# Kernel optimization log

Hardware: AMD Instinct MI355X
Metric: run time of the kernel (lower is better)

The kernel has to match this reference:

```python
import jax, jax.numpy as jnp
import numpy as np

HIDDEN = 768
HEADS = 12
HEAD_DIM = 64
SEQ = 512
DS_K = 64  # downsampling_k
EPS = 1e-6


def setup_inputs() -> dict:
    key = jax.random.key(0)
    ks = jax.random.split(key, 16)
    B = 32
    sd = 1.0 / DS_K
    glorot = jax.nn.initializers.lecun_normal()  # flax default_kernel_init
    inp = {
        "query": jax.random.normal(ks[0], (B, SEQ, HIDDEN), jnp.float32),
        "key": jax.random.normal(ks[1], (B, SEQ, HIDDEN), jnp.float32),
        "value": jax.random.normal(ks[2], (B, SEQ, HIDDEN), jnp.float32),
        "step": 0,
        # learned Linformer-style downsampling projections [k, s]
        "W_kds": sd * jax.random.normal(ks[3], (DS_K, SEQ), jnp.float32),
        "W_vds": sd * jax.random.normal(ks[4], (DS_K, SEQ), jnp.float32),
        # DenseGeneral qkv kernels [d, n, h] and biases [n, h]
        "Wq": glorot(ks[5], (HIDDEN, HEADS, HEAD_DIM), jnp.float32),
        "bq": jnp.zeros((HEADS, HEAD_DIM), jnp.float32),
        "Wk": glorot(ks[6], (HIDDEN, HEADS, HEAD_DIM), jnp.float32),
        "bk": jnp.zeros((HEADS, HEAD_DIM), jnp.float32),
        "Wv": glorot(ks[7], (HIDDEN, HEADS, HEAD_DIM), jnp.float32),
        "bv": jnp.zeros((HEADS, HEAD_DIM), jnp.float32),
        # out projection contracts (n, h) -> hidden
        "Wout": glorot(ks[8], (HEADS * HEAD_DIM, HIDDEN), jnp.float32).reshape(HEADS, HEAD_DIM, HIDDEN),
        "bout": jnp.zeros((HIDDEN,), jnp.float32),
    }
    return inp


def reference(query, key, value, step, W_kds, W_vds, Wq, bq, Wk, bk, Wv, bv, Wout, bout):
    # Linformer-style downsample of keys/values along sequence: [b,s,d] -> [b,k,d]
    key_ds = jnp.einsum("ks,bsd->bkd", W_kds, key)
    val_ds = jnp.einsum("ks,bsd->bkd", W_vds, value)

    # per-head projections
    queries = jnp.einsum("bqd,dnh->bqnh", query, Wq) + bq    # [b,q,n,h]
    keys = jnp.einsum("bkd,dnh->bknh", key_ds, Wk) + bk      # [b,k,n,h]
    values = jnp.einsum("bkd,dnh->bknh", val_ds, Wv) + bv    # [b,k,n,h]

    # kernelized linear attention with elu feature map (mask=False path)
    phi_q = jax.nn.elu(queries) + 1.0
    phi_k = jax.nn.elu(keys) + 1.0
    s = jnp.einsum("bknd,bknh->bndh", phi_k, values)          # [b,n,h,h] KV state
    z = jnp.sum(phi_k, axis=1)                                 # [b,n,h]
    qs = jnp.einsum("bqnd,bndh->bqnh", phi_q, s)
    qz = jnp.einsum("bqnd,bnd->bqn", phi_q, z) + EPS
    a_v = qs / qz[..., None]                                   # [b,q,n,h]

    out = jnp.einsum("bqnh,nhD->bqD", a_v, Wout) + bout        # [b,q,hidden]
    return out
```

## Files before the change

### kernel.cpp

```cpp
#include <hip/hip_runtime.h>

typedef unsigned short u16;
typedef u16 u16x8 __attribute__((ext_vector_type(8)));
typedef __bf16 bf16;
typedef bf16 bf16x8 __attribute__((ext_vector_type(8)));
typedef float f32x4 __attribute__((ext_vector_type(4)));

__device__ __forceinline__ float bf2f(u16 v) {
  union { unsigned u; float f; } x; x.u = ((unsigned)v) << 16; return x.f;
}
__device__ __forceinline__ u16 f2bf(float f) {
  union { float f; unsigned u; } x; x.f = f;
  unsigned u = x.u;
  u += 0x7fffu + ((u >> 16) & 1u);
  return (u16)(u >> 16);
}

#define GLDS16(g, l) __builtin_amdgcn_global_load_lds( \
    (const __attribute__((address_space(1))) unsigned int*)(const void*)(g), \
    (__attribute__((address_space(3))) unsigned int*)(void*)(l), 16, 0, 0)

__global__ __launch_bounds__(256) void prep_k(
    const float* __restrict__ Wq, const float* __restrict__ Wk,
    const float* __restrict__ Wv, const float* __restrict__ Wout,
    const float* __restrict__ query,
    const float* __restrict__ wkds, const float* __restrict__ wvds,
    const float* __restrict__ b0, const float* __restrict__ b1,
    const float* __restrict__ b2, const float* __restrict__ b3,
    u16* __restrict__ WT, u16* __restrict__ q_bf,
    u16* __restrict__ dstW, u16* __restrict__ dstB)
{
  __shared__ u16 T[64][72];
  const int blk = blockIdx.x;
  const int t = threadIdx.x;
  if (blk < 576) {
    const int bz = blk / 144, rr = blk % 144;
    const int r0 = (rr / 12) * 64, c0 = (rr % 12) * 64;
    const float* W = (bz == 0) ? Wq : (bz == 1) ? Wk : (bz == 2) ? Wv : Wout;
    u16* O = WT + (size_t)bz * 768 * 768;
    #pragma unroll
    for (int p = 0; p < 2; ++p) {
      int v = t + p * 256;
      int r = v / 8, c = (v % 8) * 8;
      f32x4 x0 = *(const f32x4*)&W[(size_t)(r0 + r) * 768 + c0 + c];
      f32x4 x1 = *(const f32x4*)&W[(size_t)(r0 + r) * 768 + c0 + c + 4];
      #pragma unroll
      for (int i = 0; i < 4; ++i) { T[r][c + i] = f2bf(x0[i]); T[r][c + 4 + i] = f2bf(x1[i]); }
    }
    __syncthreads();
    #pragma unroll
    for (int p = 0; p < 2; ++p) {
      int v = t + p * 256;
      int r = v / 8, c = (v % 8) * 8;
      u16x8 tv;
      #pragma unroll
      for (int i = 0; i < 8; ++i) tv[i] = T[c + i][r];
      *(u16x8*)&O[(size_t)(c0 + r) * 768 + r0 + c] = tv;
    }
  } else if (blk < 6720) {
    const size_t i = (size_t)(blk - 576) * 256 + t;
    f32x4 a = *(const f32x4*)&query[i * 8];
    f32x4 b = *(const f32x4*)&query[i * 8 + 4];
    u16x8 w;
    #pragma unroll
    for (int j = 0; j < 4; ++j) { w[j] = f2bf(a[j]); w[4 + j] = f2bf(b[j]); }
    *(u16x8*)&q_bf[i * 8] = w;
  } else {
    const int i = (blk - 6720) * 256 + t;
    if (i < 32768)      dstW[i] = f2bf(wkds[i]);
    else if (i < 65536) dstW[i] = f2bf(wvds[i - 32768]);
    else {
      int j = i - 65536, s = j / 768, si = j % 768;
      const float* src = (s == 0) ? b0 : (s == 1) ? b1 : (s == 2) ? b2 : b3;
      dstB[j] = f2bf(src[si]);
    }
  }
}

__global__ __launch_bounds__(256) void ds_k(
    const u16* __restrict__ Wds,
    const float* __restrict__ key, const float* __restrict__ value,
    u16* __restrict__ key_ds)
{
  __shared__ u16 Bs[2][64 * 40];
  const int pair = blockIdx.y >> 5, b = blockIdx.y & 31;
  const float* src = (pair ? value : key) + (size_t)b * 512 * 768;
  const u16* W = Wds + pair * 32768;
  u16* dst = key_ds + (size_t)pair * 1572864 + (size_t)b * 49152;
  const int nt = blockIdx.x * 64;
  const int t = threadIdx.x, wave = t >> 6, lane = t & 63;
  const int wm = (wave >> 1) * 32, wn = (wave & 1) * 32;
  const int lrow = lane & 15, quad = lane >> 4;
  const int bn = t & 63, bk8 = (t >> 6) * 8;
  const float* bcol = src + nt + bn;

  f32x4 acc[2][2] = {};
  float breg[8];
  bf16x8 av[2][2];

  #pragma unroll
  for (int i = 0; i < 8; ++i) breg[i] = bcol[(size_t)(bk8 + i) * 768];
  #pragma unroll
  for (int i = 0; i < 2; ++i)
    av[0][i] = *(const bf16x8*)&W[(size_t)(wm + i * 16 + lrow) * 512 + quad * 8];

  #pragma unroll
  for (int step = 0; step < 16; ++step) {
    const int cur = step & 1, nxt = cur ^ 1;
    u16x8 wv;
    #pragma unroll
    for (int i = 0; i < 8; ++i) wv[i] = f2bf(breg[i]);
    *(u16x8*)&Bs[cur][bn * 40 + bk8] = wv;
    if (step < 15) {
      const int k1 = (step + 1) * 32;
      #pragma unroll
      for (int i = 0; i < 8; ++i) breg[i] = bcol[(size_t)(k1 + bk8 + i) * 768];
      #pragma unroll
      for (int i = 0; i < 2; ++i)
        av[nxt][i] = *(const bf16x8*)&W[(size_t)(wm + i * 16 + lrow) * 512 + k1 + quad * 8];
    }
    __syncthreads();
    bf16x8 bv[2];
    #pragma unroll
    for (int j = 0; j < 2; ++j)
      bv[j] = *(const bf16x8*)&Bs[cur][(wn + j * 16 + lrow) * 40 + quad * 8];
    #pragma unroll
    for (int i = 0; i < 2; ++i)
      #pragma unroll
      for (int j = 0; j < 2; ++j)
        acc[i][j] = __builtin_amdgcn_mfma_f32_16x16x32_bf16(av[cur][i], bv[j], acc[i][j], 0, 0, 0);
  }

  #pragma unroll
  for (int i = 0; i < 2; ++i)
    #pragma unroll
    for (int j = 0; j < 2; ++j) {
      const int col = nt + wn + j * 16 + lrow;
      #pragma unroll
      for (int r = 0; r < 4; ++r) {
        const int row = wm + i * 16 + quad * 4 + r;
        dst[(size_t)row * 768 + col] = f2bf(acc[i][j][r]);
      }
    }
}

template<int ACT, bool OF32>
__global__ __launch_bounds__(256) void gemm97_k(
    const u16* __restrict__ A, int lda,
    const u16* __restrict__ Bt, int ldb,
    void* __restrict__ Craw, int ldc,
    const u16* __restrict__ bias, int K)
{
  __shared__ u16 As[128 * 32];
  __shared__ u16 Bs[128 * 32];
  const int mt = blockIdx.x * 128, nt = blockIdx.y * 128;
  const int t = threadIdx.x, wave = t >> 6, lane = t & 63;
  const int wm = (wave >> 1) * 64, wn = (wave & 1) * 64;
  const int lrow = lane & 15, quad = lane >> 4;
  f32x4 acc[4][4] = {};

  for (int k0 = 0; k0 < K; k0 += 32) {
    __syncthreads();
    #pragma unroll
    for (int p = 0; p < 2; ++p) {
      const int s = wave * 128 + p * 64 + lane;
      const int r = s >> 2, c = (s & 3) * 8;
      const int lb = (wave * 128 + p * 64) * 8;
      GLDS16(&A[(size_t)(mt + r) * lda + k0 + c], &As[lb]);
      GLDS16(&Bt[(size_t)(nt + r) * ldb + k0 + c], &Bs[lb]);
    }
    __syncthreads();

    bf16x8 av[4], bv[4];
    #pragma unroll
    for (int i = 0; i < 4; ++i) av[i] = *(const bf16x8*)&As[(wm + i * 16 + lrow) * 32 + quad * 8];
    #pragma unroll
    for (int j = 0; j < 4; ++j) bv[j] = *(const bf16x8*)&Bs[(wn + j * 16 + lrow) * 32 + quad * 8];
    #pragma unroll
    for (int i = 0; i < 4; ++i)
      #pragma unroll
      for (int j = 0; j < 4; ++j)
        acc[i][j] = __builtin_amdgcn_mfma_f32_16x16x32_bf16(av[i], bv[j], acc[i][j], 0, 0, 0);
  }

  #pragma unroll
  for (int i = 0; i < 4; ++i) {
    #pragma unroll
    for (int j = 0; j < 4; ++j) {
      const int col = nt + wn + j * 16 + lrow;
      const float badd = bias ? bf2f(bias[col]) : 0.0f;
      #pragma unroll
      for (int r = 0; r < 4; ++r) {
        const int row = mt + wm + i * 16 + quad * 4 + r;
        float v = acc[i][j][r] + badd;
        if constexpr (ACT == 1) v = v > 0.0f ? v + 1.0f : __expf(v);
        if constexpr (OF32) ((float*)Craw)[(size_t)row * ldc + col] = v;
        else                ((u16*)Craw)[(size_t)row * ldc + col] = f2bf(v);
      }
    }
  }
}

template<int BM, int BN, int BK, int WM, int WN>
__global__ __launch_bounds__(256) void gemmkv_k(
    const u16* __restrict__ A, int lda,
    const u16* __restrict__ B, int ldb,
    u16* __restrict__ C, int ldc,
    const u16* __restrict__ bias,
    int K,
    long long offA_b, long long offB_b, long long offC_b, long long offBias_b)
{
  constexpr int LDSK = BK + 8;
  __shared__ u16 As[BM][LDSK];
  __shared__ u16 Bs[BN][LDSK];
  const int bb = blockIdx.z;
  A += bb * offA_b; B += bb * offB_b; C += bb * offC_b; bias += bb * offBias_b;
  const int mt = blockIdx.x * BM;
  const int nt = blockIdx.y * BN;
  const int t = threadIdx.x;
  const int wave = t >> 6, lane = t & 63;
  constexpr int WAVES_N = BN / WN;
  const int wm = (wave / WAVES_N) * WM;
  const int wn = (wave % WAVES_N) * WN;
  constexpr int FM = WM / 16, FN = WN / 16;
  const int lrow = lane & 15, quad = lane >> 4;
  f32x4 acc[FM][FN] = {};

  for (int k0 = 0; k0 < K; k0 += BK) {
    __syncthreads();
    #pragma unroll
    for (int p = 0; p < (BM * BK / 8) / 256; ++p) {
      int v = t + p * 256;
      int r = v / (BK / 8), c = (v % (BK / 8)) * 8;
      *(u16x8*)&As[r][c] = *(const u16x8*)&A[(size_t)(mt + r) * lda + k0 + c];
    }
    #pragma unroll
    for (int p = 0; p < (BN * BK / 8) / 256; ++p) {
      int v = t + p * 256;
      int r = v / (BK / 8), c = (v % (BK / 8)) * 8;
      *(u16x8*)&Bs[r][c] = *(const u16x8*)&B[(size_t)(nt + r) * ldb + k0 + c];
    }
    __syncthreads();
    bf16x8 av[FM], bv[FN];
    #pragma unroll
    for (int i = 0; i < FM; ++i) av[i] = *(const bf16x8*)&As[wm + i * 16 + lrow][quad * 8];
    #pragma unroll
    for (int j = 0; j < FN; ++j) bv[j] = *(const bf16x8*)&Bs[wn + j * 16 + lrow][quad * 8];
    #pragma unroll
    for (int i = 0; i < FM; ++i)
      #pragma unroll
      for (int j = 0; j < FN; ++j)
        acc[i][j] = __builtin_amdgcn_mfma_f32_16x16x32_bf16(av[i], bv[j], acc[i][j], 0, 0, 0);
  }
  #pragma unroll
  for (int i = 0; i < FM; ++i)
    #pragma unroll
    for (int j = 0; j < FN; ++j) {
      const int col = nt + wn + j * 16 + lrow;
      const float badd = bf2f(bias[col]);
      #pragma unroll
      for (int r = 0; r < 4; ++r) {
        const int row = mt + wm + i * 16 + quad * 4 + r;
        float v = acc[i][j][r] + badd;
        if (bb == 0) v = v > 0.0f ? v + 1.0f : __expf(v);
        C[(size_t)row * ldc + col] = f2bf(v);
      }
    }
}

__global__ __launch_bounds__(256) void kv_state_k(
    const u16* __restrict__ phi_k, const u16* __restrict__ vals,
    u16* __restrict__ sT, float* __restrict__ z)
{
  __shared__ float pk[64][65];
  __shared__ float vv[64][65];
  const int x = blockIdx.x;
  const int b = x / 12, n = x % 12;
  const int t = threadIdx.x;
  const u16* pkg = phi_k + (size_t)b * 64 * 768 + n * 64;
  const u16* vvg = vals  + (size_t)b * 64 * 768 + n * 64;
  #pragma unroll
  for (int p = 0; p < 2; ++p) {
    int v = t + p * 256;
    int r = v / 8, c = (v % 8) * 8;
    u16x8 a  = *(const u16x8*)&pkg[(size_t)r * 768 + c];
    u16x8 bq = *(const u16x8*)&vvg[(size_t)r * 768 + c];
    #pragma unroll
    for (int i = 0; i < 8; ++i) { pk[r][c + i] = bf2f(a[i]); vv[r][c + i] = bf2f(bq[i]); }
  }
  __syncthreads();
  const int d0 = (t >> 4) * 4, h0 = (t & 15) * 4;
  float s4[4][4] = {};
  for (int k = 0; k < 64; ++k) {
    float pv[4], vb[4];
    #pragma unroll
    for (int i = 0; i < 4; ++i) { pv[i] = pk[k][d0 + i]; vb[i] = vv[k][h0 + i]; }
    #pragma unroll
    for (int i = 0; i < 4; ++i)
      #pragma unroll
      for (int j = 0; j < 4; ++j) s4[i][j] += pv[i] * vb[j];
  }
  const size_t base = (size_t)x * 4096;
  #pragma unroll
  for (int i = 0; i < 4; ++i)
    #pragma unroll
    for (int j = 0; j < 4; ++j)
      sT[base + (size_t)(h0 + j) * 64 + d0 + i] = f2bf(s4[i][j]);
  if (t < 64) {
    float zz = 0.f;
    for (int k = 0; k < 64; ++k) zz += pk[k][t];
    z[(size_t)x * 64 + t] = zz;
  }
}

__global__ __launch_bounds__(256) void attn_av_k(
    u16* __restrict__ phi_q, const u16* __restrict__ sT, const float* __restrict__ zbuf)
{
  __shared__ u16 As[64 * 72];
  __shared__ u16 Bs[64 * 72];
  __shared__ float zv[64];
  __shared__ float zpart[4][64];
  __shared__ float zq[64];
  const int x = blockIdx.x, y = blockIdx.y;
  const int b = y / 12, n = y % 12;
  const int t = threadIdx.x;
  u16* Abase = phi_q + (size_t)b * 512 * 768 + (size_t)x * 64 * 768 + n * 64;
  const u16* Bbase = sT + (size_t)y * 4096;
  if (t < 64) zv[t] = zbuf[(size_t)y * 64 + t];
  #pragma unroll
  for (int p = 0; p < 2; ++p) {
    int v = t + p * 256;
    int r = v >> 3, c = (v & 7) * 8;
    *(u16x8*)&As[r * 72 + c] = *(const u16x8*)&Abase[(size_t)r * 768 + c];
    *(u16x8*)&Bs[r * 72 + c] = *(const u16x8*)&Bbase[r * 64 + c];
  }
  __syncthreads();
  {
    int r = t & 63, seg = t >> 6;
    float s = 0.f;
    #pragma unroll
    for (int j = 0; j < 16; ++j) s += bf2f(As[r * 72 + seg * 16 + j]) * zv[seg * 16 + j];
    zpart[seg][r] = s;
  }
  __syncthreads();
  if (t < 64) {
    float s = zpart[0][t] + zpart[1][t] + zpart[2][t] + zpart[3][t];
    zq[t] = 1.0f / (s + 1e-6f);
  }
  const int wave = t >> 6, lane = t & 63;
  const int wm = (wave >> 1) * 32, wn = (wave & 1) * 32;
  const int lrow = lane & 15, quad = lane >> 4;
  f32x4 acc[2][2] = {};
  #pragma unroll
  for (int c = 0; c < 2; ++c) {
    bf16x8 av[2], bv[2];
    #pragma unroll
    for (int i = 0; i < 2; ++i) av[i] = *(const bf16x8*)&As[(wm + i * 16 + lrow) * 72 + c * 32 + quad * 8];
    #pragma unroll
    for (int j = 0; j < 2; ++j) bv[j] = *(const bf16x8*)&Bs[(wn + j * 16 + lrow) * 72 + c * 32 + quad * 8];
    #pragma unroll
    for (int i = 0; i < 2; ++i)
      #pragma unroll
      for (int j = 0; j < 2; ++j)
        acc[i][j] = __builtin_amdgcn_mfma_f32_16x16x32_bf16(av[i], bv[j], acc[i][j], 0, 0, 0);
  }
  __syncthreads();
  #pragma unroll
  for (int i = 0; i < 2; ++i)
    #pragma unroll
    for (int j = 0; j < 2; ++j) {
      const int col = wn + j * 16 + lrow;
      #pragma unroll
      for (int r = 0; r < 4; ++r) {
        const int row = wm + i * 16 + quad * 4 + r;
        Abase[(size_t)row * 768 + col] = f2bf(acc[i][j][r] * zq[row]);
      }
    }
}

__global__ void tagfill_k(float* out, float val, int n) {
  int i = blockIdx.x * 256 + threadIdx.x;
  if (i < n) out[i] = val;
}

extern "C" void kernel_launch(void* const* d_in, const int* in_sizes, int n_in,
                              void* d_out, int out_size, void* d_ws, size_t ws_size,
                              hipStream_t stream) {
  (void)out_size;
  float* out = (float*)d_out;

  int o;
  if (n_in >= 14 && in_sizes[3] == 1) o = 4;
  else if (n_in == 13) o = 3;
  else { tagfill_k<<<4, 256, 0, stream>>>(out, 77.0f, 1024); return; }
  if (in_sizes[0] != 12582912 || in_sizes[o + 0] != 32768 || in_sizes[o + 2] != 589824) {
    tagfill_k<<<4, 256, 0, stream>>>(out, 88.0f, 1024); return;
  }

  const float* query = (const float*)d_in[0];
  const float* key   = (const float*)d_in[1];
  const float* value = (const float*)d_in[2];
  const float* W_kds = (const float*)d_in[o + 0];
  const float* W_vds = (const float*)d_in[o + 1];
  const float* Wq   = (const float*)d_in[o + 2];
  const float* bq   = (const float*)d_in[o + 3];
  const float* Wk   = (const float*)d_in[o + 4];
  const float* bk   = (const float*)d_in[o + 5];
  const float* Wv   = (const float*)d_in[o + 6];
  const float* bv   = (const float*)d_in[o + 7];
  const float* Wout = (const float*)d_in[o + 8];
  const float* bout = (const float*)d_in[o + 9];

  const size_t NEED = 55187456;
  if (ws_size < NEED) { tagfill_k<<<4, 256, 0, stream>>>(out, 123.0f, 1024); return; }

  char* base = (char*)d_ws;
  u16*   WT     = (u16*)base;
  char*  Breg   = base + 4718592;
  u16*   q_bf   = (u16*)Breg;
  u16*   key_ds = (u16*)Breg;
  u16*   sT     = (u16*)Breg;
  float* zbuf   = (float*)(Breg + 3145728);
  u16*   phi_k  = (u16*)(Breg + 6291456);
  u16*   vals   = (u16*)(Breg + 9437184);
  u16*   phi_q  = (u16*)(base + 29884416);
  u16*   Wds_c  = (u16*)(base + 55050240);
  u16*   bias_c = (u16*)(base + 55181312);
  u16* a_v = phi_q;
  u16* WqT   = WT;
  u16* WkT   = WT + 768 * 768;
  u16* WoutT = WT + 3 * 768 * 768;
  u16* bq_c = bias_c, *bk_c = bias_c + 768, *bout_c = bias_c + 2304;

  prep_k<<<6988, 256, 0, stream>>>(Wq, Wk, Wv, Wout, query, W_kds, W_vds,
                                   bq, bk, bv, bout, WT, q_bf, Wds_c, bias_c);

  gemm97_k<1, false><<<dim3(128, 6), 256, 0, stream>>>(
      q_bf, 768, WqT, 768, phi_q, 768, bq_c, 768);

  ds_k<<<dim3(12, 64), 256, 0, stream>>>(Wds_c, key, value, key_ds);

  gemmkv_k<64, 64, 32, 32, 32><<<dim3(32, 12, 2), 256, 0, stream>>>(
      key_ds, 768, WkT, 768, phi_k, 768, bk_c, 768,
      1572864, 589824, 1572864, 768);

  kv_state_k<<<dim3(384), 256, 0, stream>>>(phi_k, vals, sT, zbuf);

  attn_av_k<<<dim3(8, 384), 256, 0, stream>>>(phi_q, sT, zbuf);

  gemm97_k<0, true><<<dim3(128, 6), 256, 0, stream>>>(
      a_v, 768, WoutT, 768, out, 768, bout_c, 768);
}
```

Before: 313.2 us.

## Fuse Linformer downsampling into prep kernel with swizzled single-stage LDS tile

```diff
diff --git a/kernel.cpp b/kernel.cpp
--- a/kernel.cpp
+++ b/kernel.cpp
@@ -20,21 +20,105 @@
     (const __attribute__((address_space(1))) unsigned int*)(const void*)(g), \
     (__attribute__((address_space(3))) unsigned int*)(void*)(l), 16, 0, 0)
 
-__global__ __launch_bounds__(256) void prep_k(
+__global__ __launch_bounds__(256, 4) void prepds_k(
     const float* __restrict__ Wq, const float* __restrict__ Wk,
     const float* __restrict__ Wv, const float* __restrict__ Wout,
     const float* __restrict__ query,
-    const float* __restrict__ wkds, const float* __restrict__ wvds,
+    const float* __restrict__ W_kds, const float* __restrict__ W_vds,
     const float* __restrict__ b0, const float* __restrict__ b1,
     const float* __restrict__ b2, const float* __restrict__ b3,
+    const float* __restrict__ key, const float* __restrict__ value,
     u16* __restrict__ WT, u16* __restrict__ q_bf,
-    u16* __restrict__ dstW, u16* __restrict__ dstB)
+    u16* __restrict__ dstB, u16* __restrict__ key_ds)
 {
-  __shared__ u16 T[64][72];
+  __shared__ u16 S[64 * 256];
   const int blk = blockIdx.x;
   const int t = threadIdx.x;
-  if (blk < 576) {
-    const int bz = blk / 144, rr = blk % 144;
+
+  if (blk < 768) {
+    const int nt = (blk % 12) * 64;
+    const int yb = blk / 12;
+    const int pair = yb >> 5, b = yb & 31;
+    const float* src = (pair ? value : key) + (size_t)b * 512 * 768;
+    const float* W32 = pair ? W_vds : W_kds;
+    u16* dst = key_ds + (size_t)pair * 1572864 + (size_t)b * 49152;
+    const int wave = t >> 6, lane = t & 63;
+    const int bn = lane;
+    const int kl = wave * 64;
+    const int sw = (bn & 7) << 3;
+    const float* bcol = src + nt + bn;
+    const int wm = (wave >> 1) * 32, wn = (wave & 1) * 32;
+    const int lrow = lane & 15, quad = lane >> 4;
+    f32x4 acc[2][2] = {};
+
+    auto st16 = [&](const float* buf, int off) {
+      #pragma unroll
+      for (int g = 0; g < 2; ++g) {
+        u16x8 wv;
+        #pragma unroll
+        for (int i = 0; i < 8; ++i) wv[i] = f2bf(buf[g * 8 + i]);
+        *(u16x8*)&S[bn * 256 + ((kl + off + g * 8) ^ sw)] = wv;
+      }
+    };
+
+    #pragma unroll
+    for (int ph = 0; ph < 2; ++ph) {
+      const int kb = ph * 256;
+      if (ph) __syncthreads();
+      float ba[16], bb[16];
+      #pragma unroll
+      for (int i = 0; i < 16; ++i) ba[i] = bcol[(size_t)(kb + kl + i) * 768];
+      #pragma unroll
+      for (int i = 0; i < 16; ++i) bb[i] = bcol[(size_t)(kb + kl + 16 + i) * 768];
+      st16(ba, 0);
+      #pragma unroll
+      for (int i = 0; i < 16; ++i) ba[i] = bcol[(size_t)(kb + kl + 32 + i) * 768];
+      st16(bb, 16);
+      #pragma unroll
+      for (int i = 0; i < 16; ++i) bb[i] = bcol[(size_t)(kb + kl + 48 + i) * 768];
+      st16(ba, 32);
+      st16(bb, 48);
+      __syncthreads();
+      #pragma unroll
+      for (int step = 0; step < 8; ++step) {
+        bf16x8 av2[2], bv[2];
+        #pragma unroll
+        for (int i = 0; i < 2; ++i) {
+          const float* wr = &W32[(size_t)(wm + i * 16 + lrow) * 512 + kb + step * 32 + quad * 8];
+          f32x4 w0 = *(const f32x4*)wr;
+          f32x4 w1 = *(const f32x4*)(wr + 4);
+          u16x8 aw;
+          #pragma unroll
+          for (int jj = 0; jj < 4; ++jj) { aw[jj] = f2bf(w0[jj]); aw[4 + jj] = f2bf(w1[jj]); }
+          av2[i] = *(bf16x8*)&aw;
+        }
+        #pragma unroll
+        for (int j = 0; j < 2; ++j) {
+          const int n = wn + j * 16 + lrow;
+          bv[j] = *(const bf16x8*)&S[n * 256 + ((step * 32 + quad * 8) ^ ((n & 7) << 3))];
+        }
+        #pragma unroll
+        for (int i = 0; i < 2; ++i)
+          #pragma unroll
+          for (int j = 0; j < 2; ++j)
+            acc[i][j] = __builtin_amdgcn_mfma_f32_16x16x32_bf16(av2[i], bv[j], acc[i][j], 0, 0, 0);
+      }
+    }
+    #pragma unroll
+    for (int i = 0; i < 2; ++i)
+      #pragma unroll
+      for (int j = 0; j < 2; ++j) {
+        const int col = nt + wn + j * 16 + lrow;
+        #pragma unroll
+        for (int r = 0; r < 4; ++r) {
+          const int row = wm + i * 16 + quad * 4 + r;
+          dst[(size_t)row * 768 + col] = f2bf(acc[i][j][r]);
+        }
+      }
+  } else if (blk < 1344) {
+    u16 (*T)[72] = (u16(*)[72])S;
+    const int tb = blk - 768;
+    const int bz = tb / 144, rr = tb % 144;
     const int r0 = (rr / 12) * 64, c0 = (rr % 12) * 64;
     const float* W = (bz == 0) ? Wq : (bz == 1) ? Wk : (bz == 2) ? Wv : Wout;
     u16* O = WT + (size_t)bz * 768 * 768;
@@ -57,8 +141,8 @@
       for (int i = 0; i < 8; ++i) tv[i] = T[c + i][r];
       *(u16x8*)&O[(size_t)(c0 + r) * 768 + r0 + c] = tv;
     }
-  } else if (blk < 6720) {
-    const size_t i = (size_t)(blk - 576) * 256 + t;
+  } else if (blk < 7488) {
+    const size_t i = (size_t)(blk - 1344) * 256 + t;
     f32x4 a = *(const f32x4*)&query[i * 8];
     f32x4 b = *(const f32x4*)&query[i * 8 + 4];
     u16x8 w;
@@ -66,82 +150,13 @@
     for (int j = 0; j < 4; ++j) { w[j] = f2bf(a[j]); w[4 + j] = f2bf(b[j]); }
     *(u16x8*)&q_bf[i * 8] = w;
   } else {
-    const int i = (blk - 6720) * 256 + t;
-    if (i < 32768)      dstW[i] = f2bf(wkds[i]);
-    else if (i < 65536) dstW[i] = f2bf(wvds[i - 32768]);
-    else {
-      int j = i - 65536, s = j / 768, si = j % 768;
+    const int i = (blk - 7488) * 256 + t;
+    if (i < 3072) {
+      int s = i / 768, si = i % 768;
       const float* src = (s == 0) ? b0 : (s == 1) ? b1 : (s == 2) ? b2 : b3;
-      dstB[j] = f2bf(src[si]);
-    }
-  }
-}
-
-__global__ __launch_bounds__(256) void ds_k(
-    const u16* __restrict__ Wds,
-    const float* __restrict__ key, const float* __restrict__ value,
-    u16* __restrict__ key_ds)
-{
-  __shared__ u16 Bs[2][64 * 40];
-  const int pair = blockIdx.y >> 5, b = blockIdx.y & 31;
-  const float* src = (pair ? value : key) + (size_t)b * 512 * 768;
-  const u16* W = Wds + pair * 32768;
-  u16* dst = key_ds + (size_t)pair * 1572864 + (size_t)b * 49152;
-  const int nt = blockIdx.x * 64;
-  const int t = threadIdx.x, wave = t >> 6, lane = t & 63;
-  const int wm = (wave >> 1) * 32, wn = (wave & 1) * 32;
-  const int lrow = lane & 15, quad = lane >> 4;
-  const int bn = t & 63, bk8 = (t >> 6) * 8;
-  const float* bcol = src + nt + bn;
-
-  f32x4 acc[2][2] = {};
-  float breg[8];
-  bf16x8 av[2][2];
-
-  #pragma unroll
-  for (int i = 0; i < 8; ++i) breg[i] = bcol[(size_t)(bk8 + i) * 768];
-  #pragma unroll
-  for (int i = 0; i < 2; ++i)
-    av[0][i] = *(const bf16x8*)&W[(size_t)(wm + i * 16 + lrow) * 512 + quad * 8];
-
-  #pragma unroll
-  for (int step = 0; step < 16; ++step) {
-    const int cur = step & 1, nxt = cur ^ 1;
-    u16x8 wv;
-    #pragma unroll
-    for (int i = 0; i < 8; ++i) wv[i] = f2bf(breg[i]);
-    *(u16x8*)&Bs[cur][bn * 40 + bk8] = wv;
-    if (step < 15) {
-      const int k1 = (step + 1) * 32;
-      #pragma unroll
-      for (int i = 0; i < 8; ++i) breg[i] = bcol[(size_t)(k1 + bk8 + i) * 768];
-      #pragma unroll
-      for (int i = 0; i < 2; ++i)
-        av[nxt][i] = *(const bf16x8*)&W[(size_t)(wm + i * 16 + lrow) * 512 + k1 + quad * 8];
-    }
-    __syncthreads();
-    bf16x8 bv[2];
-    #pragma unroll
-    for (int j = 0; j < 2; ++j)
-      bv[j] = *(const bf16x8*)&Bs[cur][(wn + j * 16 + lrow) * 40 + quad * 8];
-    #pragma unroll
-    for (int i = 0; i < 2; ++i)
-      #pragma unroll
-      for (int j = 0; j < 2; ++j)
-        acc[i][j] = __builtin_amdgcn_mfma_f32_16x16x32_bf16(av[cur][i], bv[j], acc[i][j], 0, 0, 0);
-  }
-
-  #pragma unroll
-  for (int i = 0; i < 2; ++i)
-    #pragma unroll
-    for (int j = 0; j < 2; ++j) {
-      const int col = nt + wn + j * 16 + lrow;
-      #pragma unroll
-      for (int r = 0; r < 4; ++r) {
-        const int row = wm + i * 16 + quad * 4 + r;
-        dst[(size_t)row * 768 + col] = f2bf(acc[i][j][r]);
-      }
-    }
+      dstB[i] = f2bf(src[si]);
+    }
+  }
 }
 
 template<int ACT, bool OF32>
@@ -411,34 +426,32 @@
   const float* Wout = (const float*)d_in[o + 8];
   const float* bout = (const float*)d_in[o + 9];
 
-  const size_t NEED = 55187456;
+  const size_t NEED = 61478912;
   if (ws_size < NEED) { tagfill_k<<<4, 256, 0, stream>>>(out, 123.0f, 1024); return; }
 
   char* base = (char*)d_ws;
   u16*   WT     = (u16*)base;
   char*  Breg   = base + 4718592;
   u16*   q_bf   = (u16*)Breg;
-  u16*   key_ds = (u16*)Breg;
   u16*   sT     = (u16*)Breg;
   float* zbuf   = (float*)(Breg + 3145728);
   u16*   phi_k  = (u16*)(Breg + 6291456);
   u16*   vals   = (u16*)(Breg + 9437184);
   u16*   phi_q  = (u16*)(base + 29884416);
-  u16*   Wds_c  = (u16*)(base + 55050240);
   u16*   bias_c = (u16*)(base + 55181312);
+  u16*   key_ds = (u16*)(base + 55187456);
   u16* a_v = phi_q;
   u16* WqT   = WT;
   u16* WkT   = WT + 768 * 768;
   u16* WoutT = WT + 3 * 768 * 768;
   u16* bq_c = bias_c, *bk_c = bias_c + 768, *bout_c = bias_c + 2304;
 
-  prep_k<<<6988, 256, 0, stream>>>(Wq, Wk, Wv, Wout, query, W_kds, W_vds,
-                                   bq, bk, bv, bout, WT, q_bf, Wds_c, bias_c);
+  prepds_k<<<7500, 256, 0, stream>>>(Wq, Wk, Wv, Wout, query, W_kds, W_vds,
+                                     bq, bk, bv, bout, key, value,
+                                     WT, q_bf, bias_c, key_ds);
 
   gemm97_k<1, false><<<dim3(128, 6), 256, 0, stream>>>(
       q_bf, 768, WqT, 768, phi_q, 768, bq_c, 768);
-
-  ds_k<<<dim3(12, 64), 256, 0, stream>>>(Wds_c, key, value, key_ds);
 
   gemmkv_k<64, 64, 32, 32, 32><<<dim3(32, 12, 2), 256, 0, stream>>>(
       key_ds, 768, WkT, 768, phi_k, 768, bk_c, 768,
```

Measured after the change: 316.9 us. No clear change (+1.2%).
